# Optimization experiments

Measured on AMD Instinct MI355X. Metric: run time of the kernel, lower is better.

## Reference

```python
import jax, jax.numpy as jnp
import numpy as np
import math

D_MODEL = 1024
N_HEADS = 16
D_HEAD = D_MODEL // N_HEADS
B, L = 4, 2048


def setup_inputs() -> dict:
    key = jax.random.key(0)
    ks = jax.random.split(key, 9)
    s = 1.0 / math.sqrt(D_MODEL)
    x = jax.random.normal(ks[0], (B, L, D_MODEL), dtype=jnp.float32)
    # causal mask, broadcastable over batch and heads
    attn_mask = jnp.tril(jnp.ones((L, L), dtype=jnp.int32))[None, None, :, :]
    Wq = jax.random.uniform(ks[1], (D_MODEL, D_MODEL), jnp.float32, -s, s)
    bq = jax.random.uniform(ks[2], (D_MODEL,), jnp.float32, -s, s)
    Wk = jax.random.uniform(ks[3], (D_MODEL, D_MODEL), jnp.float32, -s, s)
    bk = jax.random.uniform(ks[4], (D_MODEL,), jnp.float32, -s, s)
    Wv = jax.random.uniform(ks[5], (D_MODEL, D_MODEL), jnp.float32, -s, s)
    bv = jax.random.uniform(ks[6], (D_MODEL,), jnp.float32, -s, s)
    Wo = jax.random.uniform(ks[7], (D_MODEL, D_MODEL), jnp.float32, -s, s)
    bo = jax.random.uniform(ks[8], (D_MODEL,), jnp.float32, -s, s)
    return {"x": x, "attn_mask": attn_mask, "Wq": Wq, "bq": bq, "Wk": Wk,
            "bk": bk, "Wv": Wv, "bv": bv, "Wo": Wo, "bo": bo}


def reference(x, attn_mask, Wq, bq, Wk, bk, Wv, bv, Wo, bo):
    Bn, Ln, Dn = x.shape
    scale = 1.0 / math.sqrt(D_HEAD)

    def split_heads(t):  # [B,L,D] -> [B,H,L,dh]
        return t.reshape(Bn, Ln, N_HEADS, D_HEAD).transpose(0, 2, 1, 3)

    q = split_heads(x @ Wq + bq)
    k = split_heads(x @ Wk + bk)
    v = split_heads(x @ Wv + bv)
    scores = jnp.einsum('bhqd,bhkd->bhqk', q, k) * scale
    scores = jnp.where(attn_mask == 0, jnp.float32(-jnp.inf), scores)
    attn = jax.nn.softmax(scores, axis=-1)  # dropout p=0.0 -> identity
    ctx = jnp.einsum('bhqk,bhkd->bhqd', attn, v)
    ctx = ctx.transpose(0, 2, 1, 3).reshape(Bn, Ln, Dn)
    return ctx @ Wo + bo
```

## Files before the change

kernel.cpp:

```cpp
#include <hip/hip_runtime.h>


typedef unsigned short u16;
typedef __attribute__((ext_vector_type(8))) short short8;
typedef __attribute__((ext_vector_type(4))) float floatx4;
typedef __attribute__((ext_vector_type(2))) unsigned int uint2v;

#define NEG_BIG (-1e30f)
#define SCL_LOG2E 0.1803368801111244f

__device__ __forceinline__ u16 f2bf(float f) {
  unsigned int u = __builtin_bit_cast(unsigned int, f);
  u += 0x7fffu + ((u >> 16) & 1u);
  return (u16)(u >> 16);
}

__device__ __forceinline__ float max3f(float a, float b, float c) {
  float d;
  asm("v_max3_f32 %0, %1, %2, %3" : "=v"(d) : "v"(a), "v"(b), "v"(c));
  return d;
}

__device__ __forceinline__ short8 cvt8(const float* __restrict__ p) {
  const floatx4 a = *(const floatx4*)p;
  const floatx4 b = *(const floatx4*)(p + 4);
  short8 r;
  r[0] = (short)f2bf(a[0]); r[1] = (short)f2bf(a[1]);
  r[2] = (short)f2bf(a[2]); r[3] = (short)f2bf(a[3]);
  r[4] = (short)f2bf(b[0]); r[5] = (short)f2bf(b[1]);
  r[6] = (short)f2bf(b[2]); r[7] = (short)f2bf(b[3]);
  return r;
}

__device__ __forceinline__ void gll16(const u16* g, u16* l) {
  __builtin_amdgcn_global_load_lds((const __attribute__((address_space(1))) void*)g,
                                   (__attribute__((address_space(3))) void*)l,
                                   16, 0, 0);
}

__global__ void prep(const float* __restrict__ x, u16* __restrict__ xb,
                     const float* __restrict__ s0, const float* __restrict__ s1,
                     const float* __restrict__ s2, const float* __restrict__ s3,
                     u16* __restrict__ d0, u16* __restrict__ d1,
                     u16* __restrict__ d2, u16* __restrict__ d3) {
  const int t = threadIdx.x;
  if (blockIdx.z >= 4) {
    const int rid = (blockIdx.z - 4) * 256 + blockIdx.y * 16 + blockIdx.x;
#pragma unroll
    for (int i = 0; i < 8; ++i) {
      const size_t idx = (size_t)rid * 16384 + i * 2048 + t * 8;
      *(short8*)(xb + idx) = cvt8(x + idx);
    }
    return;
  }
  __shared__ u16 tile[64][72];
  const float* src; u16* dst;
  switch (blockIdx.z) {
    case 0: src = s0; dst = d0; break;
    case 1: src = s1; dst = d1; break;
    case 2: src = s2; dst = d2; break;
    default: src = s3; dst = d3; break;
  }
  const int c = t & 63, rg = t >> 6;
  const int x0 = blockIdx.x * 64, y0 = blockIdx.y * 64;
#pragma unroll
  for (int i = 0; i < 16; ++i) {
    const int row = rg * 16 + i;
    tile[row][c] = f2bf(src[(size_t)(y0 + row) * 1024 + x0 + c]);
  }
  __syncthreads();
#pragma unroll
  for (int i = 0; i < 16; ++i) {
    const int row = rg * 16 + i;
    dst[(size_t)(x0 + row) * 1024 + y0 + c] = tile[c][row];
  }
}

__global__ void transpose_v(const u16* __restrict__ Vb, u16* __restrict__ Vt) {
  __shared__ u16 tile[64][66];
  const int bh = blockIdx.y;
  const int l0 = blockIdx.x * 64;
  const size_t base = (size_t)bh * (2048 * 64);
  const int t = threadIdx.x;
#pragma unroll
  for (int c = t; c < 512; c += 256) {
    const int row = c >> 3, cc = c & 7;
    *(short8*)&tile[row][cc * 8] =
        *(const short8*)(Vb + base + (size_t)(l0 + row) * 64 + cc * 8);
  }
  __syncthreads();
  const int c2 = t & 63, rg = t >> 6;
#pragma unroll
  for (int i = 0; i < 16; ++i) {
    const int dr = rg * 16 + i;
    Vt[base + (size_t)dr * 2048 + l0 + c2] = tile[c2][dr];
  }
}

__global__ __launch_bounds__(256, 2) void gemm_qkv(
    const u16* __restrict__ A, const u16* __restrict__ Bt,
    const float* __restrict__ bq, const float* __restrict__ bk,
    const float* __restrict__ bv,
    u16* __restrict__ Qb, u16* __restrict__ Kb, u16* __restrict__ Vb) {
  const int K = 1024;
  __shared__ __align__(16) u16 As[128 * 32];
  __shared__ __align__(16) u16 Bs[128 * 32];
  const int t = threadIdx.x;
  const int w = t >> 6, l = t & 63;
  const int quad = l >> 4, l16 = l & 15;
  const int lin = blockIdx.y * 24 + blockIdx.x;
  const int nl = (lin & 7) * 192 + (lin >> 3);
  const int m0 = (nl / 24) * 128, n0 = (nl % 24) * 128;
  const int wr = w >> 1, wc = w & 1;

  floatx4 acc[4][4] = {};

  for (int k0 = 0; k0 < K; k0 += 32) {
    __syncthreads();
#pragma unroll
    for (int p = 0; p < 2; ++p) {
      const int c0 = (p * 4 + w) * 64;
      const int c = c0 + l;
      const int row = c >> 2;
      const int koff = (c & 3) * 8;
      gll16(A + (size_t)(m0 + row) * K + k0 + koff, &As[c0 * 8]);
      gll16(Bt + (size_t)(n0 + row) * K + k0 + koff, &Bs[c0 * 8]);
    }
    __syncthreads();

    short8 af[4], bf[4];
#pragma unroll
    for (int i = 0; i < 4; ++i)
      af[i] = *(const short8*)&As[(wr * 64 + i * 16 + l16) * 32 + quad * 8];
#pragma unroll
    for (int j = 0; j < 4; ++j)
      bf[j] = *(const short8*)&Bs[(wc * 64 + j * 16 + l16) * 32 + quad * 8];
#pragma unroll
    for (int i = 0; i < 4; ++i)
#pragma unroll
      for (int j = 0; j < 4; ++j)
        acc[i][j] = __builtin_amdgcn_mfma_f32_16x16x32_bf16(af[i], bf[j], acc[i][j], 0, 0, 0);
  }

  const int seg = n0 >> 10;
  const float* bias = (seg == 0) ? bq : (seg == 1) ? bk : bv;
  u16* dst = (seg == 0) ? Qb : (seg == 1) ? Kb : Vb;
  const float scl = (seg == 0) ? SCL_LOG2E : 1.0f;
#pragma unroll
  for (int j = 0; j < 4; ++j) {
    const int nn = (n0 & 1023) + wc * 64 + j * 16 + l16;
    const float bvs = bias[nn];
    const int h = nn >> 6, dh = nn & 63;
#pragma unroll
    for (int i = 0; i < 4; ++i) {
      const int rb = m0 + wr * 64 + i * 16 + quad * 4;
#pragma unroll
      for (int r = 0; r < 4; ++r) {
        const int m = rb + r;
        const int b = m >> 11, ll = m & 2047;
        dst[((size_t)(b * 16 + h) * 2048 + ll) * 64 + dh] = f2bf((acc[i][j][r] + bvs) * scl);
      }
    }
  }
}

__global__ __launch_bounds__(256, 2) void gemm_out(
    const u16* __restrict__ A, const u16* __restrict__ Bt,
    const float* __restrict__ bias, float* __restrict__ C, int M, int N, int K) {
  __shared__ __align__(16) u16 As[128 * 32];
  __shared__ __align__(16) u16 Bs[128 * 32];
  const int t = threadIdx.x;
  const int w = t >> 6, l = t & 63;
  const int quad = l >> 4, l16 = l & 15;
  const int lin = blockIdx.y * 8 + blockIdx.x;
  const int nl = (lin & 7) * 64 + (lin >> 3);
  const int m0 = (nl >> 3) * 128, n0 = (nl & 7) * 128;
  const int wr = w >> 1, wc = w & 1;

  floatx4 acc[4][4] = {};

  for (int k0 = 0; k0 < K; k0 += 32) {
    __syncthreads();
#pragma unroll
    for (int p = 0; p < 2; ++p) {
      const int c0 = (p * 4 + w) * 64;
      const int c = c0 + l;
      const int row = c >> 2;
      const int koff = (c & 3) * 8;
      gll16(A + (size_t)(m0 + row) * K + k0 + koff, &As[c0 * 8]);
      gll16(Bt + (size_t)(n0 + row) * K + k0 + koff, &Bs[c0 * 8]);
    }
    __syncthreads();

    short8 af[4], bf[4];
#pragma unroll
    for (int i = 0; i < 4; ++i)
      af[i] = *(const short8*)&As[(wr * 64 + i * 16 + l16) * 32 + quad * 8];
#pragma unroll
    for (int j = 0; j < 4; ++j)
      bf[j] = *(const short8*)&Bs[(wc * 64 + j * 16 + l16) * 32 + quad * 8];
#pragma unroll
    for (int i = 0; i < 4; ++i)
#pragma unroll
      for (int j = 0; j < 4; ++j)
        acc[i][j] = __builtin_amdgcn_mfma_f32_16x16x32_bf16(af[i], bf[j], acc[i][j], 0, 0, 0);
  }

#pragma unroll
  for (int j = 0; j < 4; ++j) {
    const int n = n0 + wc * 64 + j * 16 + l16;
    const float bvs = bias[n];
#pragma unroll
    for (int i = 0; i < 4; ++i) {
      const int rb = m0 + wr * 64 + i * 16 + quad * 4;
#pragma unroll
      for (int r = 0; r < 4; ++r)
        C[(size_t)(rb + r) * N + n] = acc[i][j][r] + bvs;
    }
  }
}

__global__ __launch_bounds__(512, 4) void attn_kernel(
    const u16* __restrict__ Q, const u16* __restrict__ K,
    const u16* __restrict__ Vt, u16* __restrict__ ctx) {
  __shared__ __align__(16) u16 KsA[4 * 4096];
  __shared__ __align__(16) u16 VsA[4 * 4096];
  __shared__ __align__(16) u16 Ps[8 * 16 * 64];

  const int t = threadIdx.x;
  const int w = t >> 6, l = t & 63;
  const int quad = l >> 4, l16 = l & 15;
  const int lin = blockIdx.y * 8 + blockIdx.x;
  const int bh = (lin & 7) * 8 + ((lin >> 3) & 7);
  const int pp = lin >> 6;
  const size_t base = (size_t)bh * (2048 * 64);
  const int b = bh >> 4, h = bh & 15;
  u16* Pw = &Ps[w * 16 * 64];
  unsigned int* Pw32 = (unsigned int*)Pw;

  const short8 vone = {(short)0x3F80, (short)0x3F80, (short)0x3F80, (short)0x3F80,
                       (short)0x3F80, (short)0x3F80, (short)0x3F80, (short)0x3F80};

  const int pc = w * 64 + l;
  const int sr = pc >> 3, sc = (pc & 7) ^ (sr & 7);
  const int swz = (l16 & 7);
  const int wk = w * 512;
  const u16* kg0 = K + base + (size_t)sr * 64 + sc * 8;
  const u16* vg0 = Vt + base + (size_t)sr * 2048 + sc * 8;

  auto run_seg = [&](int p) {
    const int q0 = p * 128;
    const int nkt = 2 * p + 2;
    const int qg = q0 + w * 16 + l16;
    const int qmax = q0 + w * 16 + 15;

    short8 aq[2];
#pragma unroll
    for (int ks = 0; ks < 2; ++ks)
      aq[ks] = *(const short8*)(Q + base + (size_t)qg * 64 + ks * 32 + quad * 8);

    gll16(kg0, &KsA[0 * 4096 + wk]);
    gll16(vg0, &VsA[0 * 4096 + wk]);
    gll16(kg0 + 4096, &KsA[1 * 4096 + wk]);
    gll16(vg0 + 64, &VsA[1 * 4096 + wk]);

    floatx4 o[4] = {};
    floatx4 lacc = {};
    float mrun = 0.f;
    floatx4 mneg = {};

    for (int kt = 0; kt < nkt; ++kt) {
      const int cb = (kt & 3) * 4096;
      if (kt + 2 < nkt) {
        const int nb = ((kt + 2) & 3) * 4096;
        gll16(kg0 + (size_t)(kt + 2) * 4096, &KsA[nb + wk]);
        gll16(vg0 + (kt + 2) * 64, &VsA[nb + wk]);
        asm volatile("s_waitcnt vmcnt(4)" ::: "memory");
      } else if (kt + 1 < nkt) {
        asm volatile("s_waitcnt vmcnt(2)" ::: "memory");
      } else {
        asm volatile("s_waitcnt vmcnt(0)" ::: "memory");
      }
      __builtin_amdgcn_s_barrier();

      const int kbase = kt * 64;
      if (kbase > qmax) continue;
      const bool masked = (kbase + 63 > q0 + w * 16);

      floatx4 s[4];
      __builtin_amdgcn_s_setprio(1);
#pragma unroll
      for (int tn = 0; tn < 4; ++tn) {
        const short8 bk = *(const short8*)&KsA[cb + (tn * 16 + l16) * 64 + ((quad ^ swz) << 3)];
        s[tn] = __builtin_amdgcn_mfma_f32_16x16x32_bf16(bk, aq[0], mneg, 0, 0, 0);
      }
#pragma unroll
      for (int tn = 0; tn < 4; ++tn) {
        const short8 bk = *(const short8*)&KsA[cb + (tn * 16 + l16) * 64 + (((4 + quad) ^ swz) << 3)];
        s[tn] = __builtin_amdgcn_mfma_f32_16x16x32_bf16(bk, aq[1], s[tn], 0, 0, 0);
      }
      __builtin_amdgcn_s_setprio(0);

      if (masked) {
#pragma unroll
        for (int tn = 0; tn < 4; ++tn)
#pragma unroll
          for (int r = 0; r < 4; ++r)
            if (kbase + tn * 16 + quad * 4 + r > qg) s[tn][r] = NEG_BIG;
      }
      const float m0t = max3f(s[0][0], s[0][1], s[0][2]);
      const float m1t = max3f(s[0][3], s[1][0], s[1][1]);
      const float m2t = max3f(s[1][2], s[1][3], s[2][0]);
      const float m3t = max3f(s[2][1], s[2][2], s[2][3]);
      const float m4t = max3f(s[3][0], s[3][1], s[3][2]);
      float mx = fmaxf(max3f(m0t, m1t, m2t), max3f(m3t, m4t, s[3][3]));
      mx = fmaxf(mx, __shfl_xor(mx, 16));
      mx = fmaxf(mx, __shfl_xor(mx, 32));

      if (!__all(mx <= 8.f)) {
        const float mxp = fmaxf(mx, 0.f);
        const float al = exp2f(-mxp);
        mrun += mxp;
        mneg[0] = -mrun; mneg[1] = -mrun; mneg[2] = -mrun; mneg[3] = -mrun;
#pragma unroll
        for (int tn = 0; tn < 4; ++tn)
#pragma unroll
          for (int r = 0; r < 4; ++r) s[tn][r] -= mxp;
#pragma unroll
        for (int r = 0; r < 4; ++r) lacc[r] *= al;
#pragma unroll
        for (int td = 0; td < 4; ++td)
#pragma unroll
          for (int r = 0; r < 4; ++r) o[td][r] *= al;
      }

#pragma unroll
      for (int tn = 0; tn < 4; ++tn)
#pragma unroll
        for (int r = 0; r < 4; ++r)
          s[tn][r] = exp2f(s[tn][r]);

#pragma unroll
      for (int tn = 0; tn < 4; ++tn) {
        unsigned int p0, p1;
        asm("v_cvt_pk_bf16_f32 %0, %1, %2"
            : "=v"(p0) : "v"(s[tn][0]), "v"(s[tn][1]));
        asm("v_cvt_pk_bf16_f32 %0, %1, %2"
            : "=v"(p1) : "v"(s[tn][2]), "v"(s[tn][3]));
        const int cc = (2 * tn + (quad >> 1)) ^ swz;
        uint2v pr; pr.x = p0; pr.y = p1;
        *(uint2v*)&Pw32[l16 * 32 + cc * 4 + 2 * (quad & 1)] = pr;
      }
      __asm__ volatile("s_waitcnt lgkmcnt(0)" ::: "memory");
      __builtin_amdgcn_wave_barrier();

      short8 ap[2];
#pragma unroll
      for (int ks = 0; ks < 2; ++ks)
        ap[ks] = *(const short8*)&Pw[l16 * 64 + (((ks * 4 + quad) ^ swz) << 3)];

      __builtin_amdgcn_s_setprio(1);
      lacc = __builtin_amdgcn_mfma_f32_16x16x32_bf16(vone, ap[0], lacc, 0, 0, 0);
      lacc = __builtin_amdgcn_mfma_f32_16x16x32_bf16(vone, ap[1], lacc, 0, 0, 0);
#pragma unroll
      for (int ks = 0; ks < 2; ++ks)
#pragma unroll
        for (int td = 0; td < 4; ++td) {
          const short8 bv = *(const short8*)&VsA[cb + (td * 16 + l16) * 64 + (((ks * 4 + quad) ^ swz) << 3)];
          o[td] = __builtin_amdgcn_mfma_f32_16x16x32_bf16(bv, ap[ks], o[td], 0, 0, 0);
        }
      __builtin_amdgcn_s_setprio(0);
    }

    const float inv = 1.f / lacc[0];
    u16* crow = ctx + ((size_t)(b * 2048 + qg)) * 1024 + h * 64;
#pragma unroll
    for (int td = 0; td < 4; ++td) {
      unsigned int lo, hi;
      asm("v_cvt_pk_bf16_f32 %0, %1, %2"
          : "=v"(lo) : "v"(o[td][0] * inv), "v"(o[td][1] * inv));
      asm("v_cvt_pk_bf16_f32 %0, %1, %2"
          : "=v"(hi) : "v"(o[td][2] * inv), "v"(o[td][3] * inv));
      uint2v pk;
      pk.x = lo; pk.y = hi;
      *(uint2v*)(crow + td * 16 + quad * 4) = pk;
    }
  };

  run_seg(15 - pp);
  __syncthreads();
  run_seg(pp);
}

extern "C" void kernel_launch(void* const* d_in, const int* in_sizes, int n_in,
                              void* d_out, int out_size, void* d_ws, size_t ws_size,
                              hipStream_t stream) {
  const float* x  = (const float*)d_in[0];
  const float* Wq = (const float*)d_in[2];
  const float* bq = (const float*)d_in[3];
  const float* Wk = (const float*)d_in[4];
  const float* bk = (const float*)d_in[5];
  const float* Wv = (const float*)d_in[6];
  const float* bv = (const float*)d_in[7];
  const float* Wo = (const float*)d_in[8];
  const float* bo = (const float*)d_in[9];

  u16* ws = (u16*)d_ws;
  const size_t WSZ = 1u << 20;
  const size_t TSZ = 8u << 20;
  u16* WqT = ws;
  u16* WkT = ws + WSZ;
  u16* WvT = ws + 2 * WSZ;
  u16* WoT = ws + 3 * WSZ;
  u16* xb  = ws + 4 * WSZ;
  u16* Qb  = xb + TSZ;
  u16* Kb  = Qb + TSZ;
  u16* Vb  = Kb + TSZ;
  u16* Vtb = xb;
  u16* Ctx = Vb;

  const dim3 tb(256);
  prep<<<dim3(16, 16, 6), tb, 0, stream>>>(x, xb, Wq, Wk, Wv, Wo, WqT, WkT, WvT, WoT);
  gemm_qkv<<<dim3(24, 64), tb, 0, stream>>>(xb, WqT, bq, bk, bv, Qb, Kb, Vb);
  transpose_v<<<dim3(32, 64), tb, 0, stream>>>(Vb, Vtb);
  attn_kernel<<<dim3(8, 64), dim3(512), 0, stream>>>(Qb, Kb, Vtb, Ctx);
  gemm_out<<<dim3(8, 64), tb, 0, stream>>>(Ctx, WoT, bo, (float*)d_out, 8192, 1024, 1024);
}
```

Before: 279.9 us.

## Multi-buffer GEMM shared tiles with prefetch-distance-2 async loads in QKV and output projections

Both projection GEMMs switch from a single shared-memory tile with two barriers per k-step to a 4-slot ring buffer. Global-to-LDS loads run two k-tiles ahead, and manual vmcnt waits plus one barrier per step gate each tile. The goal is to hide global-load latency behind the MFMA work and drop one barrier per iteration. Shared memory per block grows from 16 KB to 64 KB, which may limit occupancy below the 2 blocks per CU requested by the launch bounds. Correctness depends on the vmcnt counts matching the outstanding loads and on the 4-slot ring keeping a buffer from being overwritten while a slower wave still reads it.

```diff
diff --git a/kernel.cpp b/kernel.cpp
--- a/kernel.cpp
+++ b/kernel.cpp
@@ -103,8 +103,8 @@
     const float* __restrict__ bv,
     u16* __restrict__ Qb, u16* __restrict__ Kb, u16* __restrict__ Vb) {
   const int K = 1024;
-  __shared__ __align__(16) u16 As[128 * 32];
-  __shared__ __align__(16) u16 Bs[128 * 32];
+  __shared__ __align__(16) u16 AsA[4 * 4096];
+  __shared__ __align__(16) u16 BsA[4 * 4096];
   const int t = threadIdx.x;
   const int w = t >> 6, l = t & 63;
   const int quad = l >> 4, l16 = l & 15;
@@ -113,28 +113,49 @@
   const int m0 = (nl / 24) * 128, n0 = (nl % 24) * 128;
   const int wr = w >> 1, wc = w & 1;
 
+  const int c0a = w * 64, c0b = (4 + w) * 64;
+  const int ca = c0a + l, cbl = c0b + l;
+  const int rowa = ca >> 2, koffa = (ca & 3) * 8;
+  const int rowb = cbl >> 2, koffb = (cbl & 3) * 8;
+  const u16* Aga = A + (size_t)(m0 + rowa) * K + koffa;
+  const u16* Agb = A + (size_t)(m0 + rowb) * K + koffb;
+  const u16* Bga = Bt + (size_t)(n0 + rowa) * K + koffa;
+  const u16* Bgb = Bt + (size_t)(n0 + rowb) * K + koffb;
+
   floatx4 acc[4][4] = {};
 
-  for (int k0 = 0; k0 < K; k0 += 32) {
-    __syncthreads();
-#pragma unroll
-    for (int p = 0; p < 2; ++p) {
-      const int c0 = (p * 4 + w) * 64;
-      const int c = c0 + l;
-      const int row = c >> 2;
-      const int koff = (c & 3) * 8;
-      gll16(A + (size_t)(m0 + row) * K + k0 + koff, &As[c0 * 8]);
-      gll16(Bt + (size_t)(n0 + row) * K + k0 + koff, &Bs[c0 * 8]);
-    }
-    __syncthreads();
+#pragma unroll
+  for (int kt = 0; kt < 2; ++kt) {
+    gll16(Aga + kt * 32, &AsA[kt * 4096 + c0a * 8]);
+    gll16(Bga + kt * 32, &BsA[kt * 4096 + c0a * 8]);
+    gll16(Agb + kt * 32, &AsA[kt * 4096 + c0b * 8]);
+    gll16(Bgb + kt * 32, &BsA[kt * 4096 + c0b * 8]);
+  }
+
+  for (int kt = 0; kt < 32; ++kt) {
+    const int cb = (kt & 3) * 4096;
+    if (kt + 2 < 32) {
+      const int nb = ((kt + 2) & 3) * 4096;
+      const int k0 = (kt + 2) * 32;
+      gll16(Aga + k0, &AsA[nb + c0a * 8]);
+      gll16(Bga + k0, &BsA[nb + c0a * 8]);
+      gll16(Agb + k0, &AsA[nb + c0b * 8]);
+      gll16(Bgb + k0, &BsA[nb + c0b * 8]);
+      asm volatile("s_waitcnt vmcnt(8)" ::: "memory");
+    } else if (kt + 1 < 32) {
+      asm volatile("s_waitcnt vmcnt(4)" ::: "memory");
+    } else {
+      asm volatile("s_waitcnt vmcnt(0)" ::: "memory");
+    }
+    __builtin_amdgcn_s_barrier();
 
     short8 af[4], bf[4];
 #pragma unroll
     for (int i = 0; i < 4; ++i)
-      af[i] = *(const short8*)&As[(wr * 64 + i * 16 + l16) * 32 + quad * 8];
+      af[i] = *(const short8*)&AsA[cb + (wr * 64 + i * 16 + l16) * 32 + quad * 8];
 #pragma unroll
     for (int j = 0; j < 4; ++j)
-      bf[j] = *(const short8*)&Bs[(wc * 64 + j * 16 + l16) * 32 + quad * 8];
+      bf[j] = *(const short8*)&BsA[cb + (wc * 64 + j * 16 + l16) * 32 + quad * 8];
 #pragma unroll
     for (int i = 0; i < 4; ++i)
 #pragma unroll
@@ -167,8 +188,8 @@
 __global__ __launch_bounds__(256, 2) void gemm_out(
     const u16* __restrict__ A, const u16* __restrict__ Bt,
     const float* __restrict__ bias, float* __restrict__ C, int M, int N, int K) {
-  __shared__ __align__(16) u16 As[128 * 32];
-  __shared__ __align__(16) u16 Bs[128 * 32];
+  __shared__ __align__(16) u16 AsA[4 * 4096];
+  __shared__ __align__(16) u16 BsA[4 * 4096];
   const int t = threadIdx.x;
   const int w = t >> 6, l = t & 63;
   const int quad = l >> 4, l16 = l & 15;
@@ -177,28 +198,50 @@
   const int m0 = (nl >> 3) * 128, n0 = (nl & 7) * 128;
   const int wr = w >> 1, wc = w & 1;
 
+  const int c0a = w * 64, c0b = (4 + w) * 64;
+  const int ca = c0a + l, cbl = c0b + l;
+  const int rowa = ca >> 2, koffa = (ca & 3) * 8;
+  const int rowb = cbl >> 2, koffb = (cbl & 3) * 8;
+  const u16* Aga = A + (size_t)(m0 + rowa) * K + koffa;
+  const u16* Agb = A + (size_t)(m0 + rowb) * K + koffb;
+  const u16* Bga = Bt + (size_t)(n0 + rowa) * K + koffa;
+  const u16* Bgb = Bt + (size_t)(n0 + rowb) * K + koffb;
+
   floatx4 acc[4][4] = {};
 
-  for (int k0 = 0; k0 < K; k0 += 32) {
-    __syncthreads();
-#pragma unroll
-    for (int p = 0; p < 2; ++p) {
-      const int c0 = (p * 4 + w) * 64;
-      const int c = c0 + l;
-      const int row = c >> 2;
-      const int koff = (c & 3) * 8;
-      gll16(A + (size_t)(m0 + row) * K + k0 + koff, &As[c0 * 8]);
-      gll16(Bt + (size_t)(n0 + row) * K + k0 + koff, &Bs[c0 * 8]);
-    }
-    __syncthreads();
+#pragma unroll
+  for (int kt = 0; kt < 2; ++kt) {
+    gll16(Aga + kt * 32, &AsA[kt * 4096 + c0a * 8]);
+    gll16(Bga + kt * 32, &BsA[kt * 4096 + c0a * 8]);
+    gll16(Agb + kt * 32, &AsA[kt * 4096 + c0b * 8]);
+    gll16(Bgb + kt * 32, &BsA[kt * 4096 + c0b * 8]);
+  }
+
+  const int nkt = K >> 5;
+  for (int kt = 0; kt < nkt; ++kt) {
+    const int cb = (kt & 3) * 4096;
+    if (kt + 2 < nkt) {
+      const int nb = ((kt + 2) & 3) * 4096;
+      const int k0 = (kt + 2) * 32;
+      gll16(Aga + k0, &AsA[nb + c0a * 8]);
+      gll16(Bga + k0, &BsA[nb + c0a * 8]);
+      gll16(Agb + k0, &AsA[nb + c0b * 8]);
+      gll16(Bgb + k0, &BsA[nb + c0b * 8]);
+      asm volatile("s_waitcnt vmcnt(8)" ::: "memory");
+    } else if (kt + 1 < nkt) {
+      asm volatile("s_waitcnt vmcnt(4)" ::: "memory");
+    } else {
+      asm volatile("s_waitcnt vmcnt(0)" ::: "memory");
+    }
+    __builtin_amdgcn_s_barrier();
 
     short8 af[4], bf[4];
 #pragma unroll
     for (int i = 0; i < 4; ++i)
-      af[i] = *(const short8*)&As[(wr * 64 + i * 16 + l16) * 32 + quad * 8];
+      af[i] = *(const short8*)&AsA[cb + (wr * 64 + i * 16 + l16) * 32 + quad * 8];
 #pragma unroll
     for (int j = 0; j < 4; ++j)
-      bf[j] = *(const short8*)&Bs[(wc * 64 + j * 16 + l16) * 32 + quad * 8];
+      bf[j] = *(const short8*)&BsA[cb + (wc * 64 + j * 16 + l16) * 32 + quad * 8];
 #pragma unroll
     for (int i = 0; i < 4; ++i)
 #pragma unroll
```

New measurement: 277.8 us. About the same (-0.7%).
